# Performance work log

Measured on AMD Instinct MI355X. Metric: run time of the kernel, lower is better.

Reference implementation:

```python
import jax, jax.numpy as jnp
import numpy as np

NUM_GRAPHS = 1024
DIM = 64
IN_DIM = 25
PROC_STEPS = 3


def setup_inputs() -> dict:
    key = jax.random.key(0)
    ks = jax.random.split(key, 14)
    N, E = 100000, 1600000
    s = 0.1
    x = jax.random.normal(ks[0], (N, IN_DIM), jnp.float32)
    edge_index = jax.random.randint(ks[1], (2, E), 0, N, dtype=jnp.int64)
    batch = jnp.sort(jax.random.randint(ks[2], (N,), 0, NUM_GRAPHS, dtype=jnp.int64))
    return {
        "x": x,
        "edge_index": edge_index,
        "batch": batch,
        # lin0: 25 -> 64
        "lin0_W": jax.random.normal(ks[3], (IN_DIM, DIM), jnp.float32) * s,
        "lin0_b": jnp.zeros((DIM,), jnp.float32),
        # GINConv nn: 64 -> 64
        "gin_W": jax.random.normal(ks[4], (DIM, DIM), jnp.float32) * s,
        "gin_b": jnp.zeros((DIM,), jnp.float32),
        # Set2Set LSTM: input 2*dim -> hidden dim, torch gate order (i, f, g, o)
        "W_ih": jax.random.normal(ks[5], (4 * DIM, 2 * DIM), jnp.float32) * s,
        "W_hh": jax.random.normal(ks[6], (4 * DIM, DIM), jnp.float32) * s,
        "b_ih": jnp.zeros((4 * DIM,), jnp.float32),
        "b_hh": jnp.zeros((4 * DIM,), jnp.float32),
        # lin1: 128 -> 64, lin2: 64 -> 1
        "lin1_W": jax.random.normal(ks[7], (2 * DIM, DIM), jnp.float32) * s,
        "lin1_b": jnp.zeros((DIM,), jnp.float32),
        "lin2_W": jax.random.normal(ks[8], (DIM, 1), jnp.float32) * s,
        "lin2_b": jnp.zeros((1,), jnp.float32),
    }


def reference(x, edge_index, batch, lin0_W, lin0_b, gin_W, gin_b,
              W_ih, W_hh, b_ih, b_hh, lin1_W, lin1_b, lin2_W, lin2_b):
    N = x.shape[0]
    B = NUM_GRAPHS
    # lin0 + relu
    h0 = jax.nn.relu(x @ lin0_W + lin0_b)  # [N, 64]
    # GINConv (eps=0): out = nn((1+eps)*x + sum_{j in N(i)} x_j), then relu
    src, dst = edge_index[0], edge_index[1]
    aggr = jax.ops.segment_sum(h0[src], dst, num_segments=N)  # scatter-add [N, 64]
    h1 = jax.nn.relu((h0 + aggr) @ gin_W + gin_b)  # [N, 64]
    # Set2Set pooling: 3 steps of LSTM + softmax attention over each graph
    q_star = jnp.zeros((B, 2 * DIM), h1.dtype)
    h = jnp.zeros((B, DIM), h1.dtype)
    c = jnp.zeros((B, DIM), h1.dtype)
    for _ in range(PROC_STEPS):
        gates = q_star @ W_ih.T + h @ W_hh.T + b_ih + b_hh  # [B, 4*64]
        i_g, f_g, g_g, o_g = jnp.split(gates, 4, axis=-1)
        c = jax.nn.sigmoid(f_g) * c + jax.nn.sigmoid(i_g) * jnp.tanh(g_g)
        h = jax.nn.sigmoid(o_g) * jnp.tanh(c)
        q = h  # query [B, 64]
        e = jnp.sum(h1 * q[batch], axis=-1)  # [N]
        e_max = jax.ops.segment_max(e, batch, num_segments=B)
        a_un = jnp.exp(e - e_max[batch])
        denom = jax.ops.segment_sum(a_un, batch, num_segments=B)
        denom = jnp.where(denom == 0, 1.0, denom)
        a = a_un / denom[batch]  # per-graph softmax over nodes
        r = jax.ops.segment_sum(a[:, None] * h1, batch, num_segments=B)  # [B, 64]
        q_star = jnp.concatenate([q, r], axis=-1)  # [B, 128]
    out = jax.nn.relu(q_star @ lin1_W + lin1_b)
    out = out @ lin2_W + lin2_b  # [B, 1]
    return out.reshape(-1)
```

## Files before the change

### kernel.cpp

```cpp
#include <hip/hip_runtime.h>
#include <hip/hip_fp16.h>
#include <math.h>

#define DIM 64
#define IN_DIM 25
#define B_GRAPHS 1024
#define STEPS 3
#define MAXDEG 64
#define GPB 2
#define SCCAP 160
#define BSHIFT 7
#define NBUCK_MAX 1024
#define BCAP 3072
#define CHUNK_A 4096

typedef _Float16 half8 __attribute__((ext_vector_type(8)));
typedef float    f32x4 __attribute__((ext_vector_type(4)));

__device__ __forceinline__ float wave_sum(float v) {
    #pragma unroll
    for (int o = 32; o > 0; o >>= 1) v += __shfl_xor(v, o, 64);
    return v;
}

__global__ void prepA_kernel(const int* __restrict__ ei, int E,
                             int* __restrict__ gcur,
                             unsigned* __restrict__ arena, int nbuck) {
    __shared__ int hist[NBUCK_MAX];
    int tid = threadIdx.x;
    for (int t = tid; t < nbuck; t += 256) hist[t] = 0;
    __syncthreads();
    int e0 = blockIdx.x * CHUNK_A;
    int dstr[16], lofs[16];
    #pragma unroll
    for (int k = 0; k < 16; ++k) {
        int e = e0 + k * 256 + tid;
        dstr[k] = -1;
        if (e < E) {
            int d = ei[E + e];
            dstr[k] = d;
            lofs[k] = atomicAdd(&hist[d >> BSHIFT], 1);
        }
    }
    __syncthreads();
    for (int t = tid; t < nbuck; t += 256)
        hist[t] = atomicAdd(&gcur[t], hist[t]);
    __syncthreads();
    #pragma unroll
    for (int k = 0; k < 16; ++k) {
        int d = dstr[k];
        if (d >= 0) {
            int e = e0 + k * 256 + tid;
            unsigned src = (unsigned)ei[e];
            int bk = d >> BSHIFT;
            int pos = hist[bk] + lofs[k];
            if (pos < BCAP)
                arena[(size_t)bk * BCAP + pos] =
                    (src << BSHIFT) | (unsigned)(d & ((1 << BSHIFT) - 1));
        }
    }
}

__global__ void prepB_kernel(const float* __restrict__ x,
                             const float* __restrict__ W,
                             const float* __restrict__ b,
                             __half* __restrict__ h0h,
                             const int* __restrict__ batch, int N,
                             const unsigned* __restrict__ arena,
                             const int* __restrict__ gcur,
                             int* __restrict__ cnt, int* __restrict__ csr,
                             int* __restrict__ startb, int* __restrict__ endb,
                             int nbuck, int nbL) {
    int bi = blockIdx.x;
    if (bi < nbuck) {
        int tid = threadIdx.x;
        __shared__ int cur[1 << BSHIFT];
        __shared__ int stage[(1 << BSHIFT) * MAXDEG];
        for (int t = tid; t < (1 << BSHIFT); t += 256) cur[t] = 0;
        __syncthreads();
        int nE = gcur[bi];
        if (nE > BCAP) nE = BCAP;
        int base = bi << BSHIFT;
        const unsigned* ap = arena + (size_t)bi * BCAP;
        for (int i = tid; i < nE; i += 256) {
            unsigned pk = ap[i];
            int dl  = pk & ((1 << BSHIFT) - 1);
            int src = pk >> BSHIFT;
            int pos = atomicAdd(&cur[dl], 1);
            if (pos < MAXDEG) {
                int slot = (pos & 3) * 16 + (pos >> 2);
                stage[dl * MAXDEG + slot] = src;
            }
        }
        __syncthreads();
        int rows = N - base;
        if (rows > (1 << BSHIFT)) rows = 1 << BSHIFT;
        if (rows < 0) rows = 0;
        const int4* s4 = (const int4*)stage;
        int4* g4 = (int4*)(csr + (size_t)base * MAXDEG);
        for (int f = tid; f < rows * 16; f += 256) g4[f] = s4[f];
        for (int t = tid; t < rows; t += 256)
            cnt[base + t] = cur[t] < MAXDEG ? cur[t] : MAXDEG;
    } else if (bi < nbuck + nbL) {
        int grp  = threadIdx.x >> 6;
        int lane = threadIdx.x & 63;
        int n = (bi - nbuck) * 4 + grp;
        if (n >= N) return;
        float acc = b[lane];
        const float* xr = x + (size_t)n * IN_DIM;
        #pragma unroll
        for (int k = 0; k < IN_DIM; ++k)
            acc += xr[k] * W[k * DIM + lane];
        h0h[(size_t)n * DIM + lane] = __float2half(fmaxf(acc, 0.f));
    } else {
        int i = (bi - nbuck - nbL) * 256 + threadIdx.x;
        if (i >= N) return;
        int g = batch[i];
        if (i == 0) {
            startb[g] = 0;
        } else if (batch[i - 1] != g) {
            startb[g] = i;
            endb[batch[i - 1]] = i;
        }
        if (i == N - 1) endb[g] = N;
    }
}

__global__ void gin_gather_kernel(const __half* __restrict__ h0h,
                                  const int* __restrict__ cnt,
                                  const int* __restrict__ csr,
                                  const float* __restrict__ W,
                                  const float* __restrict__ bias,
                                  __half* __restrict__ h1h, int N) {
    int wid  = threadIdx.x >> 6;
    int lane = threadIdx.x & 63;
    int sub  = lane & 15;
    int quad = lane >> 4;
    int nbase = blockIdx.x * 16;
    __shared__ __align__(16) __half agg[16][72];

    half8 bfrag0, bfrag1;
    {
        int cb = wid * 16 + sub;
        #pragma unroll
        for (int j = 0; j < 8; ++j) {
            bfrag0[j] = (_Float16)W[(quad * 8 + j) * DIM + cb];
            bfrag1[j] = (_Float16)W[(32 + quad * 8 + j) * DIM + cb];
        }
    }
    float bias_l = bias[wid * 16 + sub];

    #pragma unroll
    for (int t = 0; t < 4; ++t) {
        int n = nbase + t * 4 + wid;
        if (n < N) {
            int d = cnt[n];
            const int4* crow = (const int4*)(csr + (size_t)n * MAXDEG + quad * 16);
            int4 c0 = crow[0];
            float4 a0 = {0.f, 0.f, 0.f, 0.f};
            float4 a1 = {0.f, 0.f, 0.f, 0.f};

            bool v0 = (0 + quad) < d,  v1 = (4 + quad) < d;
            bool v2 = (8 + quad) < d,  v3 = (12 + quad) < d;
            int i0 = v0 ? c0.x : 0, i1 = v1 ? c0.y : 0;
            int i2 = v2 ? c0.z : 0, i3 = v3 ? c0.w : 0;
            uint2 r0 = *(const uint2*)(h0h + (size_t)i0 * DIM + 4 * sub);
            uint2 r1 = *(const uint2*)(h0h + (size_t)i1 * DIM + 4 * sub);
            uint2 r2 = *(const uint2*)(h0h + (size_t)i2 * DIM + 4 * sub);
            uint2 r3 = *(const uint2*)(h0h + (size_t)i3 * DIM + 4 * sub);
            #define ACC8(r, v, A)                                              \
                if (v) {                                                       \
                    __half2 ua = *reinterpret_cast<__half2*>(&(r).x);          \
                    __half2 ub = *reinterpret_cast<__half2*>(&(r).y);          \
                    float2 fa = __half22float2(ua), fb = __half22float2(ub);   \
                    A.x += fa.x; A.y += fa.y; A.z += fb.x; A.w += fb.y;        \
                }
            ACC8(r0, v0, a0) ACC8(r1, v1, a1) ACC8(r2, v2, a0) ACC8(r3, v3, a1)

            if (d > 16) {
                int4 c1 = crow[1];
                bool v4 = (16 + quad) < d, v5 = (20 + quad) < d;
                bool v6 = (24 + quad) < d, v7 = (28 + quad) < d;
                int i4 = v4 ? c1.x : 0, i5 = v5 ? c1.y : 0;
                int i6 = v6 ? c1.z : 0, i7 = v7 ? c1.w : 0;
                uint2 r4 = *(const uint2*)(h0h + (size_t)i4 * DIM + 4 * sub);
                uint2 r5 = *(const uint2*)(h0h + (size_t)i5 * DIM + 4 * sub);
                uint2 r6 = *(const uint2*)(h0h + (size_t)i6 * DIM + 4 * sub);
                uint2 r7 = *(const uint2*)(h0h + (size_t)i7 * DIM + 4 * sub);
                ACC8(r4, v4, a0) ACC8(r5, v5, a1) ACC8(r6, v6, a0) ACC8(r7, v7, a1)
            }
            if (d > 32) {
                int4 c2 = crow[2];
                int4 c3 = crow[3];
                bool w0 = (32 + quad) < d, w1 = (36 + quad) < d;
                bool w2 = (40 + quad) < d, w3 = (44 + quad) < d;
                bool w4 = (48 + quad) < d, w5 = (52 + quad) < d;
                bool w6 = (56 + quad) < d, w7 = (60 + quad) < d;
                int k0 = w0 ? c2.x : 0, k1 = w1 ? c2.y : 0;
                int k2 = w2 ? c2.z : 0, k3 = w3 ? c2.w : 0;
                int k4 = w4 ? c3.x : 0, k5 = w5 ? c3.y : 0;
                int k6 = w6 ? c3.z : 0, k7 = w7 ? c3.w : 0;
                uint2 t0 = *(const uint2*)(h0h + (size_t)k0 * DIM + 4 * sub);
                uint2 t1 = *(const uint2*)(h0h + (size_t)k1 * DIM + 4 * sub);
                uint2 t2 = *(const uint2*)(h0h + (size_t)k2 * DIM + 4 * sub);
                uint2 t3 = *(const uint2*)(h0h + (size_t)k3 * DIM + 4 * sub);
                uint2 t4 = *(const uint2*)(h0h + (size_t)k4 * DIM + 4 * sub);
                uint2 t5 = *(const uint2*)(h0h + (size_t)k5 * DIM + 4 * sub);
                uint2 t6 = *(const uint2*)(h0h + (size_t)k6 * DIM + 4 * sub);
                uint2 t7 = *(const uint2*)(h0h + (size_t)k7 * DIM + 4 * sub);
                ACC8(t0, w0, a0) ACC8(t1, w1, a1) ACC8(t2, w2, a0) ACC8(t3, w3, a1)
                ACC8(t4, w4, a0) ACC8(t5, w5, a1) ACC8(t6, w6, a0) ACC8(t7, w7, a1)
            }
            #undef ACC8

            float4 a;
            a.x = a0.x + a1.x; a.y = a0.y + a1.y;
            a.z = a0.z + a1.z; a.w = a0.w + a1.w;
            a.x += __shfl_xor(a.x, 16, 64); a.y += __shfl_xor(a.y, 16, 64);
            a.z += __shfl_xor(a.z, 16, 64); a.w += __shfl_xor(a.w, 16, 64);
            a.x += __shfl_xor(a.x, 32, 64); a.y += __shfl_xor(a.y, 32, 64);
            a.z += __shfl_xor(a.z, 32, 64); a.w += __shfl_xor(a.w, 32, 64);
            if (quad == 0) {
                const __half2* p = (const __half2*)(h0h + (size_t)n * DIM + 4 * sub);
                float2 f0 = __half22float2(p[0]), f1 = __half22float2(p[1]);
                a.x += f0.x; a.y += f0.y; a.z += f1.x; a.w += f1.y;
                __half2* dp = (__half2*)&agg[t * 4 + wid][4 * sub];
                dp[0] = __floats2half2_rn(a.x, a.y);
                dp[1] = __floats2half2_rn(a.z, a.w);
            }
        }
    }
    __syncthreads();

    half8 afrag0 = *(const half8*)&agg[sub][quad * 8];
    half8 afrag1 = *(const half8*)&agg[sub][32 + quad * 8];
    f32x4 acc = {0.f, 0.f, 0.f, 0.f};
    acc = __builtin_amdgcn_mfma_f32_16x16x32_f16(afrag0, bfrag0, acc, 0, 0, 0);
    acc = __builtin_amdgcn_mfma_f32_16x16x32_f16(afrag1, bfrag1, acc, 0, 0, 0);
    #pragma unroll
    for (int r = 0; r < 4; ++r) {
        int n = nbase + quad * 4 + r;
        if (n < N) {
            float v = fmaxf(acc[r] + bias_l, 0.f);
            h1h[(size_t)n * DIM + wid * 16 + sub] = __float2half(v);
        }
    }
}

__global__ __launch_bounds__(256)
void set2set_fused_kernel(const __half* __restrict__ h1h,
                          const float* __restrict__ W_ih,
                          const float* __restrict__ W_hh,
                          const float* __restrict__ b_ih,
                          const float* __restrict__ b_hh,
                          const int* __restrict__ startb,
                          const int* __restrict__ endb,
                          const float* __restrict__ lin1_W,
                          const float* __restrict__ lin1_b,
                          const float* __restrict__ lin2_W,
                          const float* __restrict__ lin2_b,
                          float* __restrict__ out) {
    int g0  = blockIdx.x * GPB;
    int tid = threadIdx.x;
    __shared__ __align__(16) float qsbuf[GPB][2 * DIM];
    __shared__ float csbuf[GPB][DIM];
    __shared__ float gatesL[GPB][4 * DIM];
    __shared__ float scL[GPB][SCCAP];
    __shared__ float pmax[GPB][2];
    __shared__ float pden[GPB][2];
    __shared__ __align__(16) float4 pr[GPB][2][16];

    int wid  = tid >> 6;
    int myg  = wid >> 1;
    int wh   = wid & 1;
    int lane = tid & 63;
    int stg  = startb[g0 + myg];
    int cntg = endb[g0 + myg] - stg;
    if (cntg < 0) cntg = 0;

    for (int f = tid; f < GPB * 2 * DIM; f += 256) ((float*)qsbuf)[f] = 0.f;
    for (int f = tid; f < GPB * DIM; f += 256) ((float*)csbuf)[f] = 0.f;
    float bias_t = b_ih[tid] + b_hh[tid];
    __syncthreads();

    int sub   = lane & 15;
    int jslot = lane >> 4;
    int i0    = wh * 4 + jslot;

    for (int step = 0; step < STEPS; ++step) {
        {
            float a0 = bias_t, a1 = bias_t;
            const float4* wi = (const float4*)(W_ih + (size_t)tid * 2 * DIM);
            const float4* q0 = (const float4*)qsbuf[0];
            const float4* q1 = (const float4*)qsbuf[1];
            #pragma unroll 8
            for (int k = 0; k < 2 * DIM / 4; ++k) {
                float4 w = wi[k];
                float4 v0 = q0[k], v1 = q1[k];
                a0 += w.x * v0.x + w.y * v0.y + w.z * v0.z + w.w * v0.w;
                a1 += w.x * v1.x + w.y * v1.y + w.z * v1.z + w.w * v1.w;
            }
            const float4* wh4 = (const float4*)(W_hh + (size_t)tid * DIM);
            #pragma unroll 8
            for (int k = 0; k < DIM / 4; ++k) {
                float4 w = wh4[k];
                float4 v0 = q0[k], v1 = q1[k];
                a0 += w.x * v0.x + w.y * v0.y + w.z * v0.z + w.w * v0.w;
                a1 += w.x * v1.x + w.y * v1.y + w.z * v1.z + w.w * v1.w;
            }
            gatesL[0][tid] = a0; gatesL[1][tid] = a1;
        }
        __syncthreads();
        if (tid < GPB * DIM) {
            int g = tid >> 6, d = tid & 63;
            float ig = gatesL[g][d];
            float fg = gatesL[g][DIM + d];
            float gg = gatesL[g][2 * DIM + d];
            float og = gatesL[g][3 * DIM + d];
            float si = 1.f / (1.f + __expf(-ig));
            float sf = 1.f / (1.f + __expf(-fg));
            float so = 1.f / (1.f + __expf(-og));
            float cn = sf * csbuf[g][d] + si * tanhf(gg);
            float hn = so * tanhf(cn);
            csbuf[g][d] = cn;
            qsbuf[g][d] = hn;
        }
        __syncthreads();

        const float4 q4 = *(const float4*)(&qsbuf[myg][4 * sub]);

        float gmax = -INFINITY;
        for (int i = i0; i < cntg; i += 8) {
            const __half2* p =
                (const __half2*)(h1h + (size_t)(stg + i) * DIM + 4 * sub);
            float2 f0 = __half22float2(p[0]), f1 = __half22float2(p[1]);
            float pdot = f0.x * q4.x + f0.y * q4.y + f1.x * q4.z + f1.y * q4.w;
            pdot += __shfl_xor(pdot, 1, 64);
            pdot += __shfl_xor(pdot, 2, 64);
            pdot += __shfl_xor(pdot, 4, 64);
            pdot += __shfl_xor(pdot, 8, 64);
            if (sub == 0 && i < SCCAP) scL[myg][i] = pdot;
            gmax = fmaxf(gmax, pdot);
        }
        gmax = fmaxf(gmax, __shfl_xor(gmax, 16, 64));
        gmax = fmaxf(gmax, __shfl_xor(gmax, 32, 64));
        if (lane == 0) pmax[myg][wh] = gmax;
        __syncthreads();
        float m = fmaxf(pmax[myg][0], pmax[myg][1]);

        float4 racc = {0.f, 0.f, 0.f, 0.f};
        float den = 0.f;
        for (int i = i0; i < cntg; i += 8) {
            const __half2* p =
                (const __half2*)(h1h + (size_t)(stg + i) * DIM + 4 * sub);
            float2 f0 = __half22float2(p[0]), f1 = __half22float2(p[1]);
            float pdot;
            if (i < SCCAP) {
                pdot = scL[myg][i];
            } else {
                pdot = f0.x * q4.x + f0.y * q4.y + f1.x * q4.z + f1.y * q4.w;
                pdot += __shfl_xor(pdot, 1, 64);
                pdot += __shfl_xor(pdot, 2, 64);
                pdot += __shfl_xor(pdot, 4, 64);
                pdot += __shfl_xor(pdot, 8, 64);
            }
            float w = __expf(pdot - m);
            if (sub == 0) den += w;
            racc.x += w * f0.x; racc.y += w * f0.y;
            racc.z += w * f1.x; racc.w += w * f1.y;
        }
        racc.x += __shfl_xor(racc.x, 16, 64); racc.y += __shfl_xor(racc.y, 16, 64);
        racc.z += __shfl_xor(racc.z, 16, 64); racc.w += __shfl_xor(racc.w, 16, 64);
        racc.x += __shfl_xor(racc.x, 32, 64); racc.y += __shfl_xor(racc.y, 32, 64);
        racc.z += __shfl_xor(racc.z, 32, 64); racc.w += __shfl_xor(racc.w, 32, 64);
        den += __shfl_xor(den, 16, 64);
        den += __shfl_xor(den, 32, 64);
        if (jslot == 0) pr[myg][wh][sub] = racc;
        if (lane == 0) pden[myg][wh] = den;
        __syncthreads();
        if (wh == 0 && jslot == 0) {
            float4 rA = pr[myg][0][sub];
            float4 rB = pr[myg][1][sub];
            float dt = pden[myg][0] + pden[myg][1];
            if (dt == 0.f) dt = 1.f;
            float4 rv;
            rv.x = (rA.x + rB.x) / dt; rv.y = (rA.y + rB.y) / dt;
            rv.z = (rA.z + rB.z) / dt; rv.w = (rA.w + rB.w) / dt;
            *(float4*)(&qsbuf[myg][DIM + 4 * sub]) = rv;
        }
        __syncthreads();
    }

    if (wh == 0) {
        float acc = lin1_b[lane];
        const float* qv = qsbuf[myg];
        #pragma unroll 8
        for (int k = 0; k < 2 * DIM; ++k)
            acc += qv[k] * lin1_W[k * DIM + lane];
        acc = fmaxf(acc, 0.f);
        float v = acc * lin2_W[lane];
        v = wave_sum(v);
        if (lane == 0) out[g0 + myg] = v + lin2_b[0];
    }
}

extern "C" void kernel_launch(void* const* d_in, const int* in_sizes, int n_in,
                              void* d_out, int out_size, void* d_ws, size_t ws_size,
                              hipStream_t stream) {
    const float* x      = (const float*)d_in[0];
    const int*   ei     = (const int*)d_in[1];
    const int*   batch  = (const int*)d_in[2];
    const float* lin0_W = (const float*)d_in[3];
    const float* lin0_b = (const float*)d_in[4];
    const float* gin_W  = (const float*)d_in[5];
    const float* gin_b  = (const float*)d_in[6];
    const float* W_ih   = (const float*)d_in[7];
    const float* W_hh   = (const float*)d_in[8];
    const float* b_ih   = (const float*)d_in[9];
    const float* b_hh   = (const float*)d_in[10];
    const float* lin1_W = (const float*)d_in[11];
    const float* lin1_b = (const float*)d_in[12];
    const float* lin2_W = (const float*)d_in[13];
    const float* lin2_b = (const float*)d_in[14];
    float* out = (float*)d_out;

    const int N = in_sizes[2];
    const int E = in_sizes[1] / 2;

    char* ws = (char*)d_ws;
    size_t off = 0;
    auto take = [&](size_t bytes) -> char* {
        char* p = ws + off;
        off += (bytes + 255) & ~(size_t)255;
        return p;
    };
    int nbuck = (N + (1 << BSHIFT) - 1) >> BSHIFT;

    __half*   h0h   = (__half*)take((size_t)N * DIM * 2);
    __half*   h1h   = (__half*)take((size_t)N * DIM * 2);
    int*      csr   = (int*)take((size_t)N * MAXDEG * 4);
    unsigned* arena = (unsigned*)take((size_t)nbuck * BCAP * 4);
    int*      cnt   = (int*)take((size_t)N * 4);
    int* startb = (int*)take((size_t)B_GRAPHS * 4);
    int* endb   = (int*)take((size_t)B_GRAPHS * 4);
    int* gcur   = (int*)take((size_t)NBUCK_MAX * 4);
    size_t zero_bytes = (size_t)((char*)gcur - (char*)startb) + NBUCK_MAX * 4;
    hipMemsetAsync(startb, 0, zero_bytes, stream);

    int nb4   = (N + 3) / 4;
    int nb16  = (N + 15) / 16;
    int nb256 = (N + 255) / 256;
    int fillB = (E + CHUNK_A - 1) / CHUNK_A;

    hipLaunchKernelGGL(prepA_kernel, dim3(fillB), dim3(256), 0, stream,
                       ei, E, gcur, arena, nbuck);
    hipLaunchKernelGGL(prepB_kernel, dim3(nbuck + nb4 + nb256), dim3(256), 0, stream,
                       x, lin0_W, lin0_b, h0h, batch, N,
                       arena, gcur, cnt, csr, startb, endb, nbuck, nb4);
    hipLaunchKernelGGL(gin_gather_kernel, dim3(nb16), dim3(256), 0, stream,
                       h0h, cnt, csr, gin_W, gin_b, h1h, N);
    hipLaunchKernelGGL(set2set_fused_kernel, dim3(B_GRAPHS / GPB), dim3(256), 0, stream,
                       h1h, W_ih, W_hh, b_ih, b_hh, startb, endb,
                       lin1_W, lin1_b, lin2_W, lin2_b, out);
}
```

Measured before the change: 279.4 us.

## Replace CSR build and gather with per-bucket LDS atomic scatter aggregation

```diff
diff --git a/kernel.cpp b/kernel.cpp
--- a/kernel.cpp
+++ b/kernel.cpp
@@ -6,13 +6,13 @@
 #define IN_DIM 25
 #define B_GRAPHS 1024
 #define STEPS 3
-#define MAXDEG 64
 #define GPB 2
 #define SCCAP 160
 #define BSHIFT 7
 #define NBUCK_MAX 1024
 #define BCAP 3072
 #define CHUNK_A 4096
+#define ASTRIDE 68
 
 typedef _Float16 half8 __attribute__((ext_vector_type(8)));
 typedef float    f32x4 __attribute__((ext_vector_type(4)));
@@ -23,88 +23,55 @@
     return v;
 }
 
-__global__ void prepA_kernel(const int* __restrict__ ei, int E,
-                             int* __restrict__ gcur,
-                             unsigned* __restrict__ arena, int nbuck) {
-    __shared__ int hist[NBUCK_MAX];
-    int tid = threadIdx.x;
-    for (int t = tid; t < nbuck; t += 256) hist[t] = 0;
-    __syncthreads();
-    int e0 = blockIdx.x * CHUNK_A;
-    int dstr[16], lofs[16];
-    #pragma unroll
-    for (int k = 0; k < 16; ++k) {
-        int e = e0 + k * 256 + tid;
-        dstr[k] = -1;
-        if (e < E) {
-            int d = ei[E + e];
-            dstr[k] = d;
-            lofs[k] = atomicAdd(&hist[d >> BSHIFT], 1);
-        }
-    }
-    __syncthreads();
-    for (int t = tid; t < nbuck; t += 256)
-        hist[t] = atomicAdd(&gcur[t], hist[t]);
-    __syncthreads();
-    #pragma unroll
-    for (int k = 0; k < 16; ++k) {
-        int d = dstr[k];
-        if (d >= 0) {
+__global__ void prep_kernel(const float* __restrict__ x,
+                            const float* __restrict__ W,
+                            const float* __restrict__ b,
+                            __half* __restrict__ h0h,
+                            const int* __restrict__ ei, int E,
+                            const int* __restrict__ batch, int N,
+                            int* __restrict__ gcur,
+                            unsigned* __restrict__ arena,
+                            int* __restrict__ startb, int* __restrict__ endb,
+                            int fillB, int nbL, int nbuck) {
+    int bi = blockIdx.x;
+    if (bi < fillB) {
+        __shared__ int hist[NBUCK_MAX];
+        int tid = threadIdx.x;
+        for (int t = tid; t < nbuck; t += 256) hist[t] = 0;
+        __syncthreads();
+        int e0 = bi * CHUNK_A;
+        int dstr[16], lofs[16];
+        #pragma unroll
+        for (int k = 0; k < 16; ++k) {
             int e = e0 + k * 256 + tid;
-            unsigned src = (unsigned)ei[e];
-            int bk = d >> BSHIFT;
-            int pos = hist[bk] + lofs[k];
-            if (pos < BCAP)
-                arena[(size_t)bk * BCAP + pos] =
-                    (src << BSHIFT) | (unsigned)(d & ((1 << BSHIFT) - 1));
-        }
-    }
-}
-
-__global__ void prepB_kernel(const float* __restrict__ x,
-                             const float* __restrict__ W,
-                             const float* __restrict__ b,
-                             __half* __restrict__ h0h,
-                             const int* __restrict__ batch, int N,
-                             const unsigned* __restrict__ arena,
-                             const int* __restrict__ gcur,
-                             int* __restrict__ cnt, int* __restrict__ csr,
-                             int* __restrict__ startb, int* __restrict__ endb,
-                             int nbuck, int nbL) {
-    int bi = blockIdx.x;
-    if (bi < nbuck) {
-        int tid = threadIdx.x;
-        __shared__ int cur[1 << BSHIFT];
-        __shared__ int stage[(1 << BSHIFT) * MAXDEG];
-        for (int t = tid; t < (1 << BSHIFT); t += 256) cur[t] = 0;
-        __syncthreads();
-        int nE = gcur[bi];
-        if (nE > BCAP) nE = BCAP;
-        int base = bi << BSHIFT;
-        const unsigned* ap = arena + (size_t)bi * BCAP;
-        for (int i = tid; i < nE; i += 256) {
-            unsigned pk = ap[i];
-            int dl  = pk & ((1 << BSHIFT) - 1);
-            int src = pk >> BSHIFT;
-            int pos = atomicAdd(&cur[dl], 1);
-            if (pos < MAXDEG) {
-                int slot = (pos & 3) * 16 + (pos >> 2);
-                stage[dl * MAXDEG + slot] = src;
-            }
-        }
-        __syncthreads();
-        int rows = N - base;
-        if (rows > (1 << BSHIFT)) rows = 1 << BSHIFT;
-        if (rows < 0) rows = 0;
-        const int4* s4 = (const int4*)stage;
-        int4* g4 = (int4*)(csr + (size_t)base * MAXDEG);
-        for (int f = tid; f < rows * 16; f += 256) g4[f] = s4[f];
-        for (int t = tid; t < rows; t += 256)
-            cnt[base + t] = cur[t] < MAXDEG ? cur[t] : MAXDEG;
-    } else if (bi < nbuck + nbL) {
+            dstr[k] = -1;
+            if (e < E) {
+                int d = ei[E + e];
+                dstr[k] = d;
+                lofs[k] = atomicAdd(&hist[d >> BSHIFT], 1);
+            }
+        }
+        __syncthreads();
+        for (int t = tid; t < nbuck; t += 256)
+            hist[t] = atomicAdd(&gcur[t], hist[t]);
+        __syncthreads();
+        #pragma unroll
+        for (int k = 0; k < 16; ++k) {
+            int d = dstr[k];
+            if (d >= 0) {
+                int e = e0 + k * 256 + tid;
+                unsigned src = (unsigned)ei[e];
+                int bk = d >> BSHIFT;
+                int pos = hist[bk] + lofs[k];
+                if (pos < BCAP)
+                    arena[(size_t)bk * BCAP + pos] =
+                        (src << BSHIFT) | (unsigned)(d & ((1 << BSHIFT) - 1));
+            }
+        }
+    } else if (bi < fillB + nbL) {
         int grp  = threadIdx.x >> 6;
         int lane = threadIdx.x & 63;
-        int n = (bi - nbuck) * 4 + grp;
+        int n = (bi - fillB) * 4 + grp;
         if (n >= N) return;
         float acc = b[lane];
         const float* xr = x + (size_t)n * IN_DIM;
@@ -113,7 +80,7 @@
             acc += xr[k] * W[k * DIM + lane];
         h0h[(size_t)n * DIM + lane] = __float2half(fmaxf(acc, 0.f));
     } else {
-        int i = (bi - nbuck - nbL) * 256 + threadIdx.x;
+        int i = (bi - fillB - nbL) * 256 + threadIdx.x;
         if (i >= N) return;
         int g = batch[i];
         if (i == 0) {
@@ -126,18 +93,24 @@
     }
 }
 
-__global__ void gin_gather_kernel(const __half* __restrict__ h0h,
-                                  const int* __restrict__ cnt,
-                                  const int* __restrict__ csr,
+__global__ void gin_bucket_kernel(const __half* __restrict__ h0h,
+                                  const unsigned* __restrict__ arena,
+                                  const int* __restrict__ gcur,
                                   const float* __restrict__ W,
                                   const float* __restrict__ bias,
                                   __half* __restrict__ h1h, int N) {
-    int wid  = threadIdx.x >> 6;
-    int lane = threadIdx.x & 63;
+    int bk   = blockIdx.x;
+    int tid  = threadIdx.x;
+    int wid  = tid >> 6;
+    int lane = tid & 63;
     int sub  = lane & 15;
     int quad = lane >> 4;
-    int nbase = blockIdx.x * 16;
-    __shared__ __align__(16) __half agg[16][72];
+    __shared__ __align__(16) float aggr[128][ASTRIDE];
+
+    int base = bk << BSHIFT;
+    int rows = N - base;
+    if (rows > 128) rows = 128;
+    if (rows < 0) rows = 0;
 
     half8 bfrag0, bfrag1;
     {
@@ -150,99 +123,68 @@
     }
     float bias_l = bias[wid * 16 + sub];
 
+    for (int r = wid; r < rows; r += 4)
+        aggr[r][lane] = __half2float(h0h[(size_t)(base + r) * DIM + lane]);
+    __syncthreads();
+
+    int nE = gcur[bk];
+    if (nE > BCAP) nE = BCAP;
+    const unsigned* ap = arena + (size_t)bk * BCAP;
+    int per    = (nE + 3) >> 2;
+    int wstart = wid * per;
+    int wend   = wstart + per;
+    if (wend > nE) wend = nE;
+    for (int c = wstart; c < wend; c += 64) {
+        int m = wend - c;
+        if (m > 64) m = 64;
+        unsigned pk = (c + lane < wend) ? ap[c + lane] : 0u;
+        for (int j = 0; j < m; j += 8) {
+            float vals[8];
+            int   dls[8];
+            #pragma unroll
+            for (int k = 0; k < 8; ++k) {
+                unsigned p = __shfl(pk, j + k, 64);
+                bool vd = (j + k) < m;
+                int src = vd ? (int)(p >> BSHIFT) : 0;
+                dls[k] = vd ? (int)(p & ((1u << BSHIFT) - 1)) : -1;
+                vals[k] = __half2float(h0h[(size_t)src * DIM + lane]);
+            }
+            #pragma unroll
+            for (int k = 0; k < 8; ++k)
+                if (dls[k] >= 0) atomicAdd(&aggr[dls[k]][lane], vals[k]);
+        }
+    }
+    __syncthreads();
+
     #pragma unroll
-    for (int t = 0; t < 4; ++t) {
-        int n = nbase + t * 4 + wid;
-        if (n < N) {
-            int d = cnt[n];
-            const int4* crow = (const int4*)(csr + (size_t)n * MAXDEG + quad * 16);
-            int4 c0 = crow[0];
-            float4 a0 = {0.f, 0.f, 0.f, 0.f};
-            float4 a1 = {0.f, 0.f, 0.f, 0.f};
-
-            bool v0 = (0 + quad) < d,  v1 = (4 + quad) < d;
-            bool v2 = (8 + quad) < d,  v3 = (12 + quad) < d;
-            int i0 = v0 ? c0.x : 0, i1 = v1 ? c0.y : 0;
-            int i2 = v2 ? c0.z : 0, i3 = v3 ? c0.w : 0;
-            uint2 r0 = *(const uint2*)(h0h + (size_t)i0 * DIM + 4 * sub);
-            uint2 r1 = *(const uint2*)(h0h + (size_t)i1 * DIM + 4 * sub);
-            uint2 r2 = *(const uint2*)(h0h + (size_t)i2 * DIM + 4 * sub);
-            uint2 r3 = *(const uint2*)(h0h + (size_t)i3 * DIM + 4 * sub);
-            #define ACC8(r, v, A)                                              \
-                if (v) {                                                       \
-                    __half2 ua = *reinterpret_cast<__half2*>(&(r).x);          \
-                    __half2 ub = *reinterpret_cast<__half2*>(&(r).y);          \
-                    float2 fa = __half22float2(ua), fb = __half22float2(ub);   \
-                    A.x += fa.x; A.y += fa.y; A.z += fb.x; A.w += fb.y;        \
-                }
-            ACC8(r0, v0, a0) ACC8(r1, v1, a1) ACC8(r2, v2, a0) ACC8(r3, v3, a1)
-
-            if (d > 16) {
-                int4 c1 = crow[1];
-                bool v4 = (16 + quad) < d, v5 = (20 + quad) < d;
-                bool v6 = (24 + quad) < d, v7 = (28 + quad) < d;
-                int i4 = v4 ? c1.x : 0, i5 = v5 ? c1.y : 0;
-                int i6 = v6 ? c1.z : 0, i7 = v7 ? c1.w : 0;
-                uint2 r4 = *(const uint2*)(h0h + (size_t)i4 * DIM + 4 * sub);
-                uint2 r5 = *(const uint2*)(h0h + (size_t)i5 * DIM + 4 * sub);
-                uint2 r6 = *(const uint2*)(h0h + (size_t)i6 * DIM + 4 * sub);
-                uint2 r7 = *(const uint2*)(h0h + (size_t)i7 * DIM + 4 * sub);
-                ACC8(r4, v4, a0) ACC8(r5, v5, a1) ACC8(r6, v6, a0) ACC8(r7, v7, a1)
-            }
-            if (d > 32) {
-                int4 c2 = crow[2];
-                int4 c3 = crow[3];
-                bool w0 = (32 + quad) < d, w1 = (36 + quad) < d;
-                bool w2 = (40 + quad) < d, w3 = (44 + quad) < d;
-                bool w4 = (48 + quad) < d, w5 = (52 + quad) < d;
-                bool w6 = (56 + quad) < d, w7 = (60 + quad) < d;
-                int k0 = w0 ? c2.x : 0, k1 = w1 ? c2.y : 0;
-                int k2 = w2 ? c2.z : 0, k3 = w3 ? c2.w : 0;
-                int k4 = w4 ? c3.x : 0, k5 = w5 ? c3.y : 0;
-                int k6 = w6 ? c3.z : 0, k7 = w7 ? c3.w : 0;
-                uint2 t0 = *(const uint2*)(h0h + (size_t)k0 * DIM + 4 * sub);
-                uint2 t1 = *(const uint2*)(h0h + (size_t)k1 * DIM + 4 * sub);
-                uint2 t2 = *(const uint2*)(h0h + (size_t)k2 * DIM + 4 * sub);
-                uint2 t3 = *(const uint2*)(h0h + (size_t)k3 * DIM + 4 * sub);
-                uint2 t4 = *(const uint2*)(h0h + (size_t)k4 * DIM + 4 * sub);
-                uint2 t5 = *(const uint2*)(h0h + (size_t)k5 * DIM + 4 * sub);
-                uint2 t6 = *(const uint2*)(h0h + (size_t)k6 * DIM + 4 * sub);
-                uint2 t7 = *(const uint2*)(h0h + (size_t)k7 * DIM + 4 * sub);
-                ACC8(t0, w0, a0) ACC8(t1, w1, a1) ACC8(t2, w2, a0) ACC8(t3, w3, a1)
-                ACC8(t4, w4, a0) ACC8(t5, w5, a1) ACC8(t6, w6, a0) ACC8(t7, w7, a1)
-            }
-            #undef ACC8
-
-            float4 a;
-            a.x = a0.x + a1.x; a.y = a0.y + a1.y;
-            a.z = a0.z + a1.z; a.w = a0.w + a1.w;
-            a.x += __shfl_xor(a.x, 16, 64); a.y += __shfl_xor(a.y, 16, 64);
-            a.z += __shfl_xor(a.z, 16, 64); a.w += __shfl_xor(a.w, 16, 64);
-            a.x += __shfl_xor(a.x, 32, 64); a.y += __shfl_xor(a.y, 32, 64);
-            a.z += __shfl_xor(a.z, 32, 64); a.w += __shfl_xor(a.w, 32, 64);
-            if (quad == 0) {
-                const __half2* p = (const __half2*)(h0h + (size_t)n * DIM + 4 * sub);
-                float2 f0 = __half22float2(p[0]), f1 = __half22float2(p[1]);
-                a.x += f0.x; a.y += f0.y; a.z += f1.x; a.w += f1.y;
-                __half2* dp = (__half2*)&agg[t * 4 + wid][4 * sub];
-                dp[0] = __floats2half2_rn(a.x, a.y);
-                dp[1] = __floats2half2_rn(a.z, a.w);
-            }
-        }
-    }
-    __syncthreads();
-
-    half8 afrag0 = *(const half8*)&agg[sub][quad * 8];
-    half8 afrag1 = *(const half8*)&agg[sub][32 + quad * 8];
-    f32x4 acc = {0.f, 0.f, 0.f, 0.f};
-    acc = __builtin_amdgcn_mfma_f32_16x16x32_f16(afrag0, bfrag0, acc, 0, 0, 0);
-    acc = __builtin_amdgcn_mfma_f32_16x16x32_f16(afrag1, bfrag1, acc, 0, 0, 0);
-    #pragma unroll
-    for (int r = 0; r < 4; ++r) {
-        int n = nbase + quad * 4 + r;
-        if (n < N) {
-            float v = fmaxf(acc[r] + bias_l, 0.f);
-            h1h[(size_t)n * DIM + wid * 16 + sub] = __float2half(v);
+    for (int t = 0; t < 8; ++t) {
+        int r0 = t * 16;
+        if (r0 >= rows) break;
+        const float* arow0 = &aggr[r0 + sub][quad * 8];
+        half8 afrag0, afrag1;
+        {
+            f32x4 f0 = *(const f32x4*)(arow0);
+            f32x4 f1 = *(const f32x4*)(arow0 + 4);
+            f32x4 f2 = *(const f32x4*)(arow0 + 32);
+            f32x4 f3 = *(const f32x4*)(arow0 + 36);
+            #pragma unroll
+            for (int j = 0; j < 4; ++j) {
+                afrag0[j]     = (_Float16)f0[j];
+                afrag0[4 + j] = (_Float16)f1[j];
+                afrag1[j]     = (_Float16)f2[j];
+                afrag1[4 + j] = (_Float16)f3[j];
+            }
+        }
+        f32x4 acc = {0.f, 0.f, 0.f, 0.f};
+        acc = __builtin_amdgcn_mfma_f32_16x16x32_f16(afrag0, bfrag0, acc, 0, 0, 0);
+        acc = __builtin_amdgcn_mfma_f32_16x16x32_f16(afrag1, bfrag1, acc, 0, 0, 0);
+        #pragma unroll
+        for (int r = 0; r < 4; ++r) {
+            int n = base + r0 + quad * 4 + r;
+            if (n < N) {
+                float v = fmaxf(acc[r] + bias_l, 0.f);
+                h1h[(size_t)n * DIM + wid * 16 + sub] = __float2half(v);
+            }
         }
     }
 }
@@ -438,9 +380,7 @@
 
     __half*   h0h   = (__half*)take((size_t)N * DIM * 2);
     __half*   h1h   = (__half*)take((size_t)N * DIM * 2);
-    int*      csr   = (int*)take((size_t)N * MAXDEG * 4);
     unsigned* arena = (unsigned*)take((size_t)nbuck * BCAP * 4);
-    int*      cnt   = (int*)take((size_t)N * 4);
     int* startb = (int*)take((size_t)B_GRAPHS * 4);
     int* endb   = (int*)take((size_t)B_GRAPHS * 4);
     int* gcur   = (int*)take((size_t)NBUCK_MAX * 4);
@@ -448,17 +388,14 @@
     hipMemsetAsync(startb, 0, zero_bytes, stream);
 
     int nb4   = (N + 3) / 4;
-    int nb16  = (N + 15) / 16;
     int nb256 = (N + 255) / 256;
     int fillB = (E + CHUNK_A - 1) / CHUNK_A;
 
-    hipLaunchKernelGGL(prepA_kernel, dim3(fillB), dim3(256), 0, stream,
-                       ei, E, gcur, arena, nbuck);
-    hipLaunchKernelGGL(prepB_kernel, dim3(nbuck + nb4 + nb256), dim3(256), 0, stream,
-                       x, lin0_W, lin0_b, h0h, batch, N,
-                       arena, gcur, cnt, csr, startb, endb, nbuck, nb4);
-    hipLaunchKernelGGL(gin_gather_kernel, dim3(nb16), dim3(256), 0, stream,
-                       h0h, cnt, csr, gin_W, gin_b, h1h, N);
+    hipLaunchKernelGGL(prep_kernel, dim3(fillB + nb4 + nb256), dim3(256), 0, stream,
+                       x, lin0_W, lin0_b, h0h, ei, E, batch, N,
+                       gcur, arena, startb, endb, fillB, nb4, nbuck);
+    hipLaunchKernelGGL(gin_bucket_kernel, dim3(nbuck), dim3(256), 0, stream,
+                       h0h, arena, gcur, gin_W, gin_b, h1h, N);
     hipLaunchKernelGGL(set2set_fused_kernel, dim3(B_GRAPHS / GPB), dim3(256), 0, stream,
                        h1h, W_ih, W_hh, b_ih, b_hh, startb, endb,
                        lin1_W, lin1_b, lin2_W, lin2_b, out);
```

Result: slower. 921.9 us (+229.9%).
